# Optimization experiments

Measured on AMD Instinct MI355X. Metric: run time of the kernel, lower is better.

## Reference

```python
import jax, jax.numpy as jnp
import numpy as np

N, IN_F, OUT_F = 8192, 512, 256
ALPHA = 0.2  # leaky_relu negative slope
NEG_INF = -1e18


def setup_inputs() -> dict:
    key = jax.random.key(0)
    k1, k2, k3, k4 = jax.random.split(key, 4)
    h = jax.random.normal(k1, (N, IN_F), dtype=jnp.float32)
    adj = jax.random.randint(k2, (N, N), 0, 2, dtype=jnp.int32)
    # W: Linear(in_features, out_features, bias=False); stored [in, out] for x @ W
    lim_w = float(np.sqrt(6.0 / (IN_F + OUT_F)))
    W = jax.random.uniform(k3, (IN_F, OUT_F), minval=-lim_w, maxval=lim_w, dtype=jnp.float32)
    # a_T: Linear(2*out_features, 1); split into a1 (for H1=Wh_i) and a2 (for H2=Wh_j)
    lim_a = float(np.sqrt(6.0 / (2 * OUT_F + 1)))
    a = jax.random.uniform(k4, (2 * OUT_F,), minval=-lim_a, maxval=lim_a, dtype=jnp.float32)
    a1, a2 = a[:OUT_F], a[OUT_F:]
    return {"h": h, "adj": adj, "W": W, "a1": a1, "a2": a2}


def reference(h, adj, W, a1, a2):
    Wh = h @ W  # [N, F]
    # e_ij = leaky_relu(a . [Wh_i, Wh_j]) = leaky_relu(Wh_i.a1 + Wh_j.a2)
    # (mathematically identical to repeat+cat+linear, without the [N,N,2F] tensor)
    src = Wh @ a1  # [N]
    dst = Wh @ a2  # [N]
    e = jax.nn.leaky_relu(src[:, None] + dst[None, :], negative_slope=ALPHA)  # [N, N]
    masked_e = jnp.where(adj > 0, e, jnp.float32(NEG_INF))
    attn = jax.nn.softmax(masked_e, axis=-1)  # [N, N]
    h_prime = attn @ Wh  # [N, F]
    return jax.nn.elu(h_prime)
```

## Files before the change

### kernel.cpp

```cpp
#include <hip/hip_runtime.h>
#include <hip/hip_bf16.h>

#define NN 8192
#define KIN 512
#define KOUT 256
#define ALPHA 0.2f
#define BK 64
#define ROWS 128
#define KQ (NN / 4)
#define NT4 (KQ / BK)

typedef __bf16 bf16x8 __attribute__((ext_vector_type(8)));
typedef float f32x4 __attribute__((ext_vector_type(4)));
typedef unsigned short ushort8_t __attribute__((ext_vector_type(8)));
typedef unsigned short ushort4_t __attribute__((ext_vector_type(4)));
typedef int int4v __attribute__((ext_vector_type(4)));

__device__ __forceinline__ float lrelu(float x) { return x > 0.f ? x : ALPHA * x; }

__device__ __forceinline__ unsigned short f2bf(float f) {
  union { float f; unsigned u; } v; v.f = f;
  unsigned r = v.u + 0x7fffu + ((v.u >> 16) & 1u);
  return (unsigned short)(r >> 16);
}

__device__ __forceinline__ unsigned cvt_pk_bf16(float lo, float hi) {
  unsigned r;
  asm("v_cvt_pk_bf16_f32 %0, %1, %2" : "=v"(r) : "v"(lo), "v"(hi));
  return r;
}

__global__ __launch_bounds__(512) void k_wh(const float* __restrict__ h,
                                            const float* __restrict__ W,
                                            const float* __restrict__ a1,
                                            const float* __restrict__ a2,
                                            unsigned short* __restrict__ WhB,
                                            float* __restrict__ src,
                                            float* __restrict__ dstv) {
  __shared__ float sA[16][36];
  __shared__ float sB[16][260];
  const int tid = threadIdx.x;
  const int wave = tid >> 6;
  const int lane = tid & 63;
  const int bm = blockIdx.x * 32;
  const int arow = tid >> 4;
  const int akk = tid & 15;
  const int bkr = tid >> 5;
  const int bc = (tid & 31) * 8;
  float acc[4][4] = {};
  for (int k0 = 0; k0 < KIN; k0 += 16) {
    float av = h[(size_t)(bm + arow) * KIN + k0 + akk];
    const float4* wp = (const float4*)(W + (size_t)(k0 + bkr) * KOUT + bc);
    float4 w0 = wp[0], w1 = wp[1];
    __syncthreads();
    sA[akk][arow] = av;
    *(float4*)&sB[bkr][bc] = w0;
    *(float4*)&sB[bkr][bc + 4] = w1;
    __syncthreads();
#pragma unroll
    for (int k = 0; k < 16; ++k) {
      float4 a4 = *(const float4*)&sA[k][wave * 4];
      float4 b4 = *(const float4*)&sB[k][lane * 4];
      float aa[4] = {a4.x, a4.y, a4.z, a4.w};
      float bb[4] = {b4.x, b4.y, b4.z, b4.w};
#pragma unroll
      for (int i = 0; i < 4; ++i)
#pragma unroll
        for (int jj = 0; jj < 4; ++jj)
          acc[i][jj] = fmaf(aa[i], bb[jj], acc[i][jj]);
    }
  }
  float4 a1v = *(const float4*)(a1 + lane * 4);
  float4 a2v = *(const float4*)(a2 + lane * 4);
  float sp[4], dp[4];
#pragma unroll
  for (int i = 0; i < 4; ++i) {
    sp[i] = acc[i][0] * a1v.x + acc[i][1] * a1v.y + acc[i][2] * a1v.z + acc[i][3] * a1v.w;
    dp[i] = acc[i][0] * a2v.x + acc[i][1] * a2v.y + acc[i][2] * a2v.z + acc[i][3] * a2v.w;
  }
#pragma unroll
  for (int off = 32; off >= 1; off >>= 1) {
#pragma unroll
    for (int i = 0; i < 4; ++i) {
      sp[i] += __shfl_xor(sp[i], off);
      dp[i] += __shfl_xor(dp[i], off);
    }
  }
  if (lane == 0) {
#pragma unroll
    for (int i = 0; i < 4; ++i) {
      src[bm + wave * 4 + i] = sp[i];
      dstv[bm + wave * 4 + i] = dp[i];
    }
  }
#pragma unroll
  for (int i = 0; i < 4; ++i) {
    ushort4_t pk;
#pragma unroll
    for (int jj = 0; jj < 4; ++jj) pk[jj] = f2bf(acc[i][jj]);
    *(ushort4_t*)(WhB + (size_t)(bm + wave * 4 + i) * KOUT + lane * 4) = pk;
  }
}

__global__ __launch_bounds__(256) void k_trF(const unsigned short* __restrict__ WhB,
                                             unsigned short* __restrict__ WhF) {
  __shared__ unsigned int sX[64][65];
  const int t = threadIdx.x;
  const int r0 = (blockIdx.x & 127) * 64;
  const int c0 = (blockIdx.x >> 7) * 64;
  const int rr = t >> 2;
  const int cq = (t & 3) * 16;
  const ushort8_t* p = (const ushort8_t*)(WhB + (size_t)(r0 + rr) * KOUT + c0 + cq);
  ushort8_t v0 = p[0], v1 = p[1];
#pragma unroll
  for (int i = 0; i < 8; ++i) {
    sX[rr][cq + i] = v0[i];
    sX[rr][cq + 8 + i] = v1[i];
  }
  __syncthreads();
  const int wv = t >> 6;
  const int lane = t & 63;
  const int q = lane >> 4;
  const int fr = lane & 15;
  const int kt = r0 >> 6;
  const int wbase = c0 >> 5;
#pragma unroll
  for (int i = 0; i < 2; ++i) {
    const int g = wv * 2 + i;
    const int wloc = g >> 2;
    const int nc = (g >> 1) & 1;
    const int kh = g & 1;
    const int j0 = kh * 32 + q * 8;
    const int lc = wloc * 32 + nc * 16 + fr;
    ushort8_t o;
#pragma unroll
    for (int e = 0; e < 8; ++e) o[e] = (unsigned short)sX[j0 + e][lc];
    const int w = wbase + wloc;
    const size_t idx = ((((size_t)kt * 8 + w) * 2 + nc) * 2 + kh) * 64 + lane;
    *(ushort8_t*)(WhF + idx * 8) = o;
  }
}

__global__ __launch_bounds__(256) void k_dmax(const float* __restrict__ dstv,
                                              float* __restrict__ Dp) {
  __shared__ float red[256];
  const int t = threadIdx.x;
  float m = -3e38f;
  for (int i = t; i < NN; i += 256) m = fmaxf(m, dstv[i]);
  red[t] = m;
  __syncthreads();
  for (int s = 128; s >= 1; s >>= 1) {
    if (t < s) red[t] = fmaxf(red[t], red[t + s]);
    __syncthreads();
  }
  if (t == 0) *Dp = red[0];
}

struct Bset { ushort8_t b[2][2]; };

#define MF(a, b, c) __builtin_amdgcn_mfma_f32_16x16x32_bf16(a, b, c, 0, 0, 0)

#define BAR()                                              \
  {                                                        \
    asm volatile("s_waitcnt lgkmcnt(0)" ::: "memory");     \
    __builtin_amdgcn_s_barrier();                          \
    asm volatile("" ::: "memory");                         \
  }

#define TI(t) (((t) + ph0) & (NT4 - 1))

#define LOADB(BS, ktl)                                                 \
  {                                                                    \
    const unsigned short* p_ = bfw + (size_t)(ktl) * 16384;            \
    BS.b[0][0] = *(const ushort8_t*)(p_);                              \
    BS.b[0][1] = *(const ushort8_t*)(p_ + 512);                        \
    BS.b[1][0] = *(const ushort8_t*)(p_ + 1024);                       \
    BS.b[1][1] = *(const ushort8_t*)(p_ + 1536);                       \
  }

#define WGEN4(AJ, ktl, koff, buf)                                      \
  {                                                                    \
    float4 dv = *(const float4*)&sD[(ktl) * BK + (koff)];              \
    float x0 = s_r + dv.x, x1 = s_r + dv.y;                            \
    float x2 = s_r + dv.z, x3 = s_r + dv.w;                            \
    float w0 = (AJ.x > 0) ? __expf(fmaxf(x0, ALPHA * x0) - c_r) : 0.f; \
    float w1 = (AJ.y > 0) ? __expf(fmaxf(x1, ALPHA * x1) - c_r) : 0.f; \
    float w2 = (AJ.z > 0) ? __expf(fmaxf(x2, ALPHA * x2) - c_r) : 0.f; \
    float w3 = (AJ.w > 0) ? __expf(fmaxf(x3, ALPHA * x3) - c_r) : 0.f; \
    lsum += (w0 + w1) + (w2 + w3);                                     \
    uint2 pk;                                                          \
    pk.x = cvt_pk_bf16(w0, w1);                                        \
    pk.y = cvt_pk_bf16(w2, w3);                                        \
    *(uint2*)(sAb + (buf) * 16384 +                                    \
              ((pr * 128 + (koff) * 2) ^ ((pr & 7) << 4))) = pk;       \
  }

#define WGEN16(A0, A1, A2, A3, ktl, buf)                               \
  {                                                                    \
    WGEN4(A0, ktl, pk16 + 0, buf);                                     \
    WGEN4(A1, ktl, pk16 + 4, buf);                                     \
    WGEN4(A2, ktl, pk16 + 8, buf);                                     \
    WGEN4(A3, ktl, pk16 + 12, buf);                                    \
  }

#define LOADADJ16(A0, A1, A2, A3, ktl)                                 \
  {                                                                    \
    const int4v* ap = (const int4v*)(adjp + (size_t)(ktl) * BK);       \
    A0 = __builtin_nontemporal_load(ap);                               \
    A1 = __builtin_nontemporal_load(ap + 1);                           \
    A2 = __builtin_nontemporal_load(ap + 2);                           \
    A3 = __builtin_nontemporal_load(ap + 3);                           \
  }

#define LDA(cur, mr, kk)                                                        \
  __builtin_bit_cast(bf16x8,                                                    \
    *(const ushort8_t*)(sAb + (cur) * 16384 +                                   \
      ((((mr) * 16 + fr) * 128 + (kk) * 64 + fq * 16) ^ ((fr & 7) << 4))))

#define MSTEP(cur, BS)                                                 \
  {                                                                    \
    _Pragma("unroll")                                                  \
    for (int mr = 0; mr < 8; ++mr) {                                   \
      bf16x8 a0 = LDA(cur, mr, 0), a1 = LDA(cur, mr, 1);               \
      acc[mr][0] = MF(a0, BS.b[0][0], acc[mr][0]);                     \
      acc[mr][0] = MF(a1, BS.b[0][1], acc[mr][0]);                     \
      acc[mr][1] = MF(a0, BS.b[1][0], acc[mr][1]);                     \
      acc[mr][1] = MF(a1, BS.b[1][1], acc[mr][1]);                     \
    }                                                                  \
  }

__global__ __launch_bounds__(1024) void k_attn(const int* __restrict__ adj,
                                               const unsigned short* __restrict__ WhF,
                                               const float* __restrict__ src,
                                               const float* __restrict__ dstv,
                                               const float* __restrict__ Dp,
                                               float* __restrict__ Pbuf,
                                               float* __restrict__ Lsum) {
  __shared__ unsigned short sA[2][ROWS][BK];
  __shared__ float sD[KQ];
  char* sAb = (char*)&sA[0][0][0];
  const int tid = threadIdx.x;
  const int lane = tid & 63;
  const int wave = tid >> 6;
  const int qtr = blockIdx.x & 3;
  const int rg = blockIdx.x >> 2;
  const int r0 = rg * ROWS;
  const int ph0 = rg & (NT4 - 1);
  const int kbase = qtr * KQ;
  const float D = *Dp;

  *(float2*)&sD[tid * 2] = *(const float2*)(dstv + kbase + tid * 2);
  __syncthreads();

  const int ptid = tid - 512;
  const int pr = ptid >> 2;
  const int pk16 = (ptid & 3) * 16;
  const float s_r = src[r0 + pr];
  const float c_r = lrelu(s_r + D);
  const int* adjp = adj + (size_t)(r0 + pr) * NN + kbase + pk16;
  float lsum = 0.f;

  const int fr = lane & 15;
  const int fq = lane >> 4;
  const unsigned short* bfw =
      WhF + ((size_t)(qtr * NT4) * 8 + wave) * 2048 + lane * 8;
  f32x4 acc[8][2];
#pragma unroll
  for (int mr = 0; mr < 8; ++mr) {
    acc[mr][0] = (f32x4){0.f, 0.f, 0.f, 0.f};
    acc[mr][1] = (f32x4){0.f, 0.f, 0.f, 0.f};
  }
  Bset B0, B1;
  int4v aA0, aA1, aA2, aA3;
  int4v aB0, aB1, aB2, aB3;

  if (wave >= 8) {
    int4v d0, d1, d2, d3;
    {
      const int4v* ap = (const int4v*)(adjp + (size_t)TI(0) * BK);
      d0 = ap[0]; d1 = ap[1]; d2 = ap[2]; d3 = ap[3];
    }
    WGEN16(d0, d1, d2, d3, TI(0), 0);
    LOADADJ16(aB0, aB1, aB2, aB3, TI(1));
    LOADADJ16(aA0, aA1, aA2, aA3, TI(2));
  } else {
    LOADB(B0, TI(0));
    LOADB(B1, TI(1));
  }
  BAR();

  if (wave < 8) {
#pragma unroll 1
    for (int p = 0; p < NT4; p += 2) {
      { MSTEP(0, B0); LOADB(B0, TI(p + 2)); BAR(); }
      { MSTEP(1, B1); LOADB(B1, TI(p + 3)); BAR(); }
    }
#pragma unroll
    for (int mr = 0; mr < 8; ++mr) {
#pragma unroll
      for (int r = 0; r < 4; ++r) {
        const int row = mr * 16 + fq * 4 + r;
#pragma unroll
        for (int nc = 0; nc < 2; ++nc) {
          const int col = wave * 32 + nc * 16 + fr;
          Pbuf[(size_t)(qtr * NN + r0 + row) * KOUT + col] = acc[mr][nc][r];
        }
      }
    }
  } else {
#pragma unroll 1
    for (int p = 0; p < NT4; p += 2) {
      {
        WGEN16(aB0, aB1, aB2, aB3, TI(p + 1), 1);
        LOADADJ16(aB0, aB1, aB2, aB3, TI(p + 3));
        BAR();
      }
      {
        if (p + 2 < NT4) { WGEN16(aA0, aA1, aA2, aA3, TI(p + 2), 0); }
        LOADADJ16(aA0, aA1, aA2, aA3, TI(p + 4));
        BAR();
      }
    }
    lsum += __shfl_xor(lsum, 1, 4);
    lsum += __shfl_xor(lsum, 2, 4);
    if ((ptid & 3) == 0) Lsum[qtr * NN + r0 + pr] = lsum;
  }
}

__global__ __launch_bounds__(256) void k_comb(const float* __restrict__ Pbuf,
                                              const float* __restrict__ Lsum,
                                              float* __restrict__ out) {
  const int t = threadIdx.x;
  const int row = blockIdx.x * 4 + (t >> 6);
  const int col = (t & 63) * 4;
  const float l = Lsum[row] + Lsum[NN + row] + Lsum[2 * NN + row] + Lsum[3 * NN + row];
  float4 p0 = *(const float4*)(Pbuf + (size_t)row * KOUT + col);
  float4 p1 = *(const float4*)(Pbuf + (size_t)(NN + row) * KOUT + col);
  float4 p2 = *(const float4*)(Pbuf + (size_t)(2 * NN + row) * KOUT + col);
  float4 p3 = *(const float4*)(Pbuf + (size_t)(3 * NN + row) * KOUT + col);
  float4 v;
  v.x = (p0.x + p1.x + p2.x + p3.x) / l;
  v.y = (p0.y + p1.y + p2.y + p3.y) / l;
  v.z = (p0.z + p1.z + p2.z + p3.z) / l;
  v.w = (p0.w + p1.w + p2.w + p3.w) / l;
  v.x = v.x > 0.f ? v.x : __expf(v.x) - 1.f;
  v.y = v.y > 0.f ? v.y : __expf(v.y) - 1.f;
  v.z = v.z > 0.f ? v.z : __expf(v.z) - 1.f;
  v.w = v.w > 0.f ? v.w : __expf(v.w) - 1.f;
  *(float4*)(out + (size_t)row * KOUT + col) = v;
}

extern "C" void kernel_launch(void* const* d_in, const int* in_sizes, int n_in,
                              void* d_out, int out_size, void* d_ws, size_t ws_size,
                              hipStream_t stream) {
  const float* h = (const float*)d_in[0];
  const int* adj = (const int*)d_in[1];
  const float* W = (const float*)d_in[2];
  const float* a1 = (const float*)d_in[3];
  const float* a2 = (const float*)d_in[4];
  float* out = (float*)d_out;

  unsigned short* WhB = (unsigned short*)d_ws;
  unsigned short* WhF = WhB + (size_t)NN * KOUT;
  float* src = (float*)(WhF + (size_t)NN * KOUT);
  float* dstv = src + NN;
  float* Dp = dstv + NN;
  float* Pbuf = Dp + 16;
  float* Lsum = Pbuf + (size_t)4 * NN * KOUT;

  hipLaunchKernelGGL(k_wh, dim3(NN / 32), dim3(512), 0, stream, h, W, a1, a2, WhB, src, dstv);
  hipLaunchKernelGGL(k_trF, dim3(512), dim3(256), 0, stream, WhB, WhF);
  hipLaunchKernelGGL(k_dmax, dim3(1), dim3(256), 0, stream, dstv, Dp);
  hipLaunchKernelGGL(k_attn, dim3(256), dim3(1024), 0, stream, adj, WhF, src, dstv, Dp, Pbuf, Lsum);
  hipLaunchKernelGGL(k_comb, dim3(NN / 4), dim3(256), 0, stream, Pbuf, Lsum, out);
}
```

Measured before the change: 150.0 us.

## Factor softmax exponent into per-column and per-row terms; halve attention block size

The per-element exp(lrelu(s+d)-c) becomes max(exp(d)*exp(s-c), exp(alpha*d)*exp(alpha*s-c)). The per-column exponentials are precomputed into shared memory and the per-row factors into registers, so the inner weight generation needs only multiplies and a max instead of a transcendental per element. The block also shrinks from 1024 to 512 threads: 4 MFMA waves each own 64 output columns and 4 producer waves each handle 32 adjacent columns per row, with launch bounds asking for 2 blocks per CU. This trades more registers per wave and possible overflow or precision differences in the factored exponentials (exp(d) could overflow for large d) for less SFU work.

```diff
diff --git a/kernel.cpp b/kernel.cpp
--- a/kernel.cpp
+++ b/kernel.cpp
@@ -156,7 +156,7 @@
   if (t == 0) *Dp = red[0];
 }
 
-struct Bset { ushort8_t b[2][2]; };
+struct Bset { ushort8_t b[4][2]; };
 
 #define MF(a, b, c) __builtin_amdgcn_mfma_f32_16x16x32_bf16(a, b, c, 0, 0, 0)
 
@@ -176,17 +176,20 @@
     BS.b[0][1] = *(const ushort8_t*)(p_ + 512);                        \
     BS.b[1][0] = *(const ushort8_t*)(p_ + 1024);                       \
     BS.b[1][1] = *(const ushort8_t*)(p_ + 1536);                       \
+    BS.b[2][0] = *(const ushort8_t*)(p_ + 2048);                       \
+    BS.b[2][1] = *(const ushort8_t*)(p_ + 2560);                       \
+    BS.b[3][0] = *(const ushort8_t*)(p_ + 3072);                       \
+    BS.b[3][1] = *(const ushort8_t*)(p_ + 3584);                       \
   }
 
 #define WGEN4(AJ, ktl, koff, buf)                                      \
   {                                                                    \
-    float4 dv = *(const float4*)&sD[(ktl) * BK + (koff)];              \
-    float x0 = s_r + dv.x, x1 = s_r + dv.y;                            \
-    float x2 = s_r + dv.z, x3 = s_r + dv.w;                            \
-    float w0 = (AJ.x > 0) ? __expf(fmaxf(x0, ALPHA * x0) - c_r) : 0.f; \
-    float w1 = (AJ.y > 0) ? __expf(fmaxf(x1, ALPHA * x1) - c_r) : 0.f; \
-    float w2 = (AJ.z > 0) ? __expf(fmaxf(x2, ALPHA * x2) - c_r) : 0.f; \
-    float w3 = (AJ.w > 0) ? __expf(fmaxf(x3, ALPHA * x3) - c_r) : 0.f; \
+    float4 e1 = *(const float4*)&sE1[(ktl) * BK + (koff)];             \
+    float4 e2 = *(const float4*)&sE2[(ktl) * BK + (koff)];             \
+    float w0 = (AJ.x > 0) ? fmaxf(e1.x * F1, e2.x * F2) : 0.f;         \
+    float w1 = (AJ.y > 0) ? fmaxf(e1.y * F1, e2.y * F2) : 0.f;         \
+    float w2 = (AJ.z > 0) ? fmaxf(e1.z * F1, e2.z * F2) : 0.f;         \
+    float w3 = (AJ.w > 0) ? fmaxf(e1.w * F1, e2.w * F2) : 0.f;         \
     lsum += (w0 + w1) + (w2 + w3);                                     \
     uint2 pk;                                                          \
     pk.x = cvt_pk_bf16(w0, w1);                                        \
@@ -195,21 +198,17 @@
               ((pr * 128 + (koff) * 2) ^ ((pr & 7) << 4))) = pk;       \
   }
 
-#define WGEN16(A0, A1, A2, A3, ktl, buf)                               \
-  {                                                                    \
-    WGEN4(A0, ktl, pk16 + 0, buf);                                     \
-    WGEN4(A1, ktl, pk16 + 4, buf);                                     \
-    WGEN4(A2, ktl, pk16 + 8, buf);                                     \
-    WGEN4(A3, ktl, pk16 + 12, buf);                                    \
-  }
-
-#define LOADADJ16(A0, A1, A2, A3, ktl)                                 \
+#define WGEN32(R, ktl, buf)                                            \
+  {                                                                    \
+    _Pragma("unroll")                                                  \
+    for (int q = 0; q < 8; ++q) { WGEN4(R[q], ktl, pk32 + q * 4, buf); } \
+  }
+
+#define LOADADJ32(R, ktl)                                              \
   {                                                                    \
     const int4v* ap = (const int4v*)(adjp + (size_t)(ktl) * BK);       \
-    A0 = __builtin_nontemporal_load(ap);                               \
-    A1 = __builtin_nontemporal_load(ap + 1);                           \
-    A2 = __builtin_nontemporal_load(ap + 2);                           \
-    A3 = __builtin_nontemporal_load(ap + 3);                           \
+    _Pragma("unroll")                                                  \
+    for (int q = 0; q < 8; ++q) { R[q] = __builtin_nontemporal_load(ap + q); } \
   }
 
 #define LDA(cur, mr, kk)                                                        \
@@ -222,22 +221,24 @@
     _Pragma("unroll")                                                  \
     for (int mr = 0; mr < 8; ++mr) {                                   \
       bf16x8 a0 = LDA(cur, mr, 0), a1 = LDA(cur, mr, 1);               \
-      acc[mr][0] = MF(a0, BS.b[0][0], acc[mr][0]);                     \
-      acc[mr][0] = MF(a1, BS.b[0][1], acc[mr][0]);                     \
-      acc[mr][1] = MF(a0, BS.b[1][0], acc[mr][1]);                     \
-      acc[mr][1] = MF(a1, BS.b[1][1], acc[mr][1]);                     \
+      _Pragma("unroll")                                                \
+      for (int nc = 0; nc < 4; ++nc) {                                 \
+        acc[mr][nc] = MF(a0, BS.b[nc][0], acc[mr][nc]);                \
+        acc[mr][nc] = MF(a1, BS.b[nc][1], acc[mr][nc]);                \
+      }                                                                \
     }                                                                  \
   }
 
-__global__ __launch_bounds__(1024) void k_attn(const int* __restrict__ adj,
-                                               const unsigned short* __restrict__ WhF,
-                                               const float* __restrict__ src,
-                                               const float* __restrict__ dstv,
-                                               const float* __restrict__ Dp,
-                                               float* __restrict__ Pbuf,
-                                               float* __restrict__ Lsum) {
+__global__ __launch_bounds__(512, 2) void k_attn(const int* __restrict__ adj,
+                                                 const unsigned short* __restrict__ WhF,
+                                                 const float* __restrict__ src,
+                                                 const float* __restrict__ dstv,
+                                                 const float* __restrict__ Dp,
+                                                 float* __restrict__ Pbuf,
+                                                 float* __restrict__ Lsum) {
   __shared__ unsigned short sA[2][ROWS][BK];
-  __shared__ float sD[KQ];
+  __shared__ float sE1[KQ];
+  __shared__ float sE2[KQ];
   char* sAb = (char*)&sA[0][0][0];
   const int tid = threadIdx.x;
   const int lane = tid & 63;
@@ -249,51 +250,60 @@
   const int kbase = qtr * KQ;
   const float D = *Dp;
 
-  *(float2*)&sD[tid * 2] = *(const float2*)(dstv + kbase + tid * 2);
+  {
+    float4 d4 = *(const float4*)(dstv + kbase + tid * 4);
+    float4 t1, t2;
+    t1.x = __expf(d4.x); t1.y = __expf(d4.y); t1.z = __expf(d4.z); t1.w = __expf(d4.w);
+    t2.x = __expf(ALPHA * d4.x); t2.y = __expf(ALPHA * d4.y);
+    t2.z = __expf(ALPHA * d4.z); t2.w = __expf(ALPHA * d4.w);
+    *(float4*)&sE1[tid * 4] = t1;
+    *(float4*)&sE2[tid * 4] = t2;
+  }
   __syncthreads();
 
-  const int ptid = tid - 512;
-  const int pr = ptid >> 2;
-  const int pk16 = (ptid & 3) * 16;
+  const int ptid = tid - 256;
+  const int pr = ptid >> 1;
+  const int pk32 = (ptid & 1) * 32;
   const float s_r = src[r0 + pr];
   const float c_r = lrelu(s_r + D);
-  const int* adjp = adj + (size_t)(r0 + pr) * NN + kbase + pk16;
+  const float F1 = __expf(s_r - c_r);
+  const float F2 = __expf(ALPHA * s_r - c_r);
+  const int* adjp = adj + (size_t)(r0 + pr) * NN + kbase + pk32;
   float lsum = 0.f;
 
   const int fr = lane & 15;
   const int fq = lane >> 4;
   const unsigned short* bfw =
-      WhF + ((size_t)(qtr * NT4) * 8 + wave) * 2048 + lane * 8;
-  f32x4 acc[8][2];
-#pragma unroll
-  for (int mr = 0; mr < 8; ++mr) {
-    acc[mr][0] = (f32x4){0.f, 0.f, 0.f, 0.f};
-    acc[mr][1] = (f32x4){0.f, 0.f, 0.f, 0.f};
-  }
+      WhF + ((size_t)(qtr * NT4) * 8 + wave * 2) * 2048 + lane * 8;
+  f32x4 acc[8][4];
+#pragma unroll
+  for (int mr = 0; mr < 8; ++mr)
+#pragma unroll
+    for (int nc = 0; nc < 4; ++nc) acc[mr][nc] = (f32x4){0.f, 0.f, 0.f, 0.f};
   Bset B0, B1;
-  int4v aA0, aA1, aA2, aA3;
-  int4v aB0, aB1, aB2, aB3;
-
-  if (wave >= 8) {
-    int4v d0, d1, d2, d3;
+  int4v aA[8], aB[8];
+
+  if (wave >= 4) {
+    int4v d[8];
     {
       const int4v* ap = (const int4v*)(adjp + (size_t)TI(0) * BK);
-      d0 = ap[0]; d1 = ap[1]; d2 = ap[2]; d3 = ap[3];
-    }
-    WGEN16(d0, d1, d2, d3, TI(0), 0);
-    LOADADJ16(aB0, aB1, aB2, aB3, TI(1));
-    LOADADJ16(aA0, aA1, aA2, aA3, TI(2));
+#pragma unroll
+      for (int q = 0; q < 8; ++q) d[q] = ap[q];
+    }
+    WGEN32(d, TI(0), 0);
+    LOADADJ32(aB, TI(1));
+    LOADADJ32(aA, TI(2));
   } else {
     LOADB(B0, TI(0));
     LOADB(B1, TI(1));
   }
   BAR();
 
-  if (wave < 8) {
+  if (wave < 4) {
 #pragma unroll 1
     for (int p = 0; p < NT4; p += 2) {
-      { MSTEP(0, B0); LOADB(B0, TI(p + 2)); BAR(); }
-      { MSTEP(1, B1); LOADB(B1, TI(p + 3)); BAR(); }
+      { MSTEP(0, B0); LOADB(B0, TI(p + 2 < NT4 ? p + 2 : NT4 - 1)); BAR(); }
+      { MSTEP(1, B1); LOADB(B1, TI(p + 3 < NT4 ? p + 3 : NT4 - 1)); BAR(); }
     }
 #pragma unroll
     for (int mr = 0; mr < 8; ++mr) {
@@ -301,8 +311,8 @@
       for (int r = 0; r < 4; ++r) {
         const int row = mr * 16 + fq * 4 + r;
 #pragma unroll
-        for (int nc = 0; nc < 2; ++nc) {
-          const int col = wave * 32 + nc * 16 + fr;
+        for (int nc = 0; nc < 4; ++nc) {
+          const int col = wave * 64 + nc * 16 + fr;
           Pbuf[(size_t)(qtr * NN + r0 + row) * KOUT + col] = acc[mr][nc][r];
         }
       }
@@ -311,19 +321,18 @@
 #pragma unroll 1
     for (int p = 0; p < NT4; p += 2) {
       {
-        WGEN16(aB0, aB1, aB2, aB3, TI(p + 1), 1);
-        LOADADJ16(aB0, aB1, aB2, aB3, TI(p + 3));
+        WGEN32(aB, TI(p + 1), 1);
+        LOADADJ32(aB, TI(p + 3 < NT4 ? p + 3 : NT4 - 1));
         BAR();
       }
       {
-        if (p + 2 < NT4) { WGEN16(aA0, aA1, aA2, aA3, TI(p + 2), 0); }
-        LOADADJ16(aA0, aA1, aA2, aA3, TI(p + 4));
+        if (p + 2 < NT4) { WGEN32(aA, TI(p + 2), 0); }
+        LOADADJ32(aA, TI(p + 4 < NT4 ? p + 4 : NT4 - 1));
         BAR();
       }
     }
-    lsum += __shfl_xor(lsum, 1, 4);
-    lsum += __shfl_xor(lsum, 2, 4);
-    if ((ptid & 3) == 0) Lsum[qtr * NN + r0 + pr] = lsum;
+    lsum += __shfl_xor(lsum, 1, 2);
+    if ((ptid & 1) == 0) Lsum[qtr * NN + r0 + pr] = lsum;
   }
 }
 
@@ -371,6 +380,6 @@
   hipLaunchKernelGGL(k_wh, dim3(NN / 32), dim3(512), 0, stream, h, W, a1, a2, WhB, src, dstv);
   hipLaunchKernelGGL(k_trF, dim3(512), dim3(256), 0, stream, WhB, WhF);
   hipLaunchKernelGGL(k_dmax, dim3(1), dim3(256), 0, stream, dstv, Dp);
-  hipLaunchKernelGGL(k_attn, dim3(256), dim3(1024), 0, stream, adj, WhF, src, dstv, Dp, Pbuf, Lsum);
+  hipLaunchKernelGGL(k_attn, dim3(256), dim3(512), 0, stream, adj, WhF, src, dstv, Dp, Pbuf, Lsum);
   hipLaunchKernelGGL(k_comb, dim3(NN / 4), dim3(256), 0, stream, Pbuf, Lsum, out);
 }
```

Measured after the change: 193.7 us. +29.2%, slower.

## Move Wh projection to bf16 MFMA and fold attention scores and max into it

Applied to the files above, without the earlier changes.

Replaces the scalar-FMA fp32 h@W kernel with an MFMA bf16 GEMM. W is pre-converted to bf16 in fragment layout, and h is converted on the fly into swizzled shared memory. The src/dst scores are computed as h·(W a1) and h·(W a2) from small precomputed vectors. The global max of dst is taken with an order-preserving atomicMax, which removes the single-block k_dmax reduction kernel. This trades extra bf16 rounding of h and W for lower compute time in the projection stage, and adds two small prep kernels.

```diff
diff --git a/kernel.cpp b/kernel.cpp
--- a/kernel.cpp
+++ b/kernel.cpp
@@ -13,7 +13,6 @@
 typedef __bf16 bf16x8 __attribute__((ext_vector_type(8)));
 typedef float f32x4 __attribute__((ext_vector_type(4)));
 typedef unsigned short ushort8_t __attribute__((ext_vector_type(8)));
-typedef unsigned short ushort4_t __attribute__((ext_vector_type(4)));
 typedef int int4v __attribute__((ext_vector_type(4)));
 
 __device__ __forceinline__ float lrelu(float x) { return x > 0.f ? x : ALPHA * x; }
@@ -30,75 +29,171 @@
   return r;
 }
 
-__global__ __launch_bounds__(512) void k_wh(const float* __restrict__ h,
-                                            const float* __restrict__ W,
+__device__ __forceinline__ unsigned fkey(float x) {
+  unsigned b = __float_as_uint(x);
+  return (b & 0x80000000u) ? ~b : (b | 0x80000000u);
+}
+__device__ __forceinline__ float funkey(unsigned k) {
+  unsigned b = (k & 0x80000000u) ? (k ^ 0x80000000u) : ~k;
+  return __uint_as_float(b);
+}
+
+#define MF(a, b, c) __builtin_amdgcn_mfma_f32_16x16x32_bf16(a, b, c, 0, 0, 0)
+
+__global__ __launch_bounds__(256) void k_wa(const float* __restrict__ W,
                                             const float* __restrict__ a1,
                                             const float* __restrict__ a2,
-                                            unsigned short* __restrict__ WhB,
-                                            float* __restrict__ src,
-                                            float* __restrict__ dstv) {
-  __shared__ float sA[16][36];
-  __shared__ float sB[16][260];
+                                            float* __restrict__ Wa1,
+                                            float* __restrict__ Wa2,
+                                            unsigned* __restrict__ Dup) {
+  const int k = blockIdx.x * 256 + threadIdx.x;
+  float s1 = 0.f, s2 = 0.f;
+  const float* wr = W + (size_t)k * KOUT;
+  for (int c = 0; c < KOUT; c += 4) {
+    float4 w4 = *(const float4*)(wr + c);
+    float4 b1 = *(const float4*)(a1 + c);
+    float4 b2 = *(const float4*)(a2 + c);
+    s1 += w4.x * b1.x + w4.y * b1.y + w4.z * b1.z + w4.w * b1.w;
+    s2 += w4.x * b2.x + w4.y * b2.y + w4.z * b2.z + w4.w * b2.w;
+  }
+  Wa1[k] = s1;
+  Wa2[k] = s2;
+  if (k == 0) *Dup = 0u;
+}
+
+__global__ __launch_bounds__(64) void k_prep(const float* __restrict__ W,
+                                             unsigned short* __restrict__ Wb) {
+  const int b = blockIdx.x;
+  const int kt = b >> 4, cg = b & 15;
+  const int l = threadIdx.x;
+  const int krow = kt * 32 + (l >> 4) * 8;
+  const int col = cg * 16 + (l & 15);
+  ushort8_t o;
+#pragma unroll
+  for (int e = 0; e < 8; ++e) o[e] = f2bf(W[(size_t)(krow + e) * KOUT + col]);
+  *(ushort8_t*)(Wb + ((size_t)b * 64 + l) * 8) = o;
+}
+
+__global__ __launch_bounds__(512) void k_wh2(const float* __restrict__ h,
+                                             const unsigned short* __restrict__ Wb,
+                                             const float* __restrict__ Wa1,
+                                             const float* __restrict__ Wa2,
+                                             unsigned short* __restrict__ WhB,
+                                             float* __restrict__ src,
+                                             float* __restrict__ dstv,
+                                             unsigned* __restrict__ Dup) {
+  __shared__ unsigned short sH[64][64];
+  __shared__ unsigned short sBounce[64][128];
+  __shared__ float sW1[KIN], sW2[KIN];
+  char* sHb = (char*)&sH[0][0];
   const int tid = threadIdx.x;
-  const int wave = tid >> 6;
   const int lane = tid & 63;
-  const int bm = blockIdx.x * 32;
-  const int arow = tid >> 4;
-  const int akk = tid & 15;
-  const int bkr = tid >> 5;
-  const int bc = (tid & 31) * 8;
-  float acc[4][4] = {};
-  for (int k0 = 0; k0 < KIN; k0 += 16) {
-    float av = h[(size_t)(bm + arow) * KIN + k0 + akk];
-    const float4* wp = (const float4*)(W + (size_t)(k0 + bkr) * KOUT + bc);
-    float4 w0 = wp[0], w1 = wp[1];
+  const int wv = tid >> 6;
+  const int r0 = blockIdx.x * 64;
+  const int fr = lane & 15, fq = lane >> 4;
+
+  sW1[tid] = Wa1[tid];
+  sW2[tid] = Wa2[tid];
+
+  const int srow = tid >> 3;
+  const int skc = (tid & 7) * 8;
+  const float* hp = h + (size_t)(r0 + srow) * KIN + skc;
+  const int wby = ((srow * 128 + skc * 2) ^ ((srow & 7) << 4));
+  float sp = 0.f, dp = 0.f;
+
+  f32x4 acc[4][2];
+#pragma unroll
+  for (int mr = 0; mr < 4; ++mr) {
+    acc[mr][0] = (f32x4){0.f, 0.f, 0.f, 0.f};
+    acc[mr][1] = (f32x4){0.f, 0.f, 0.f, 0.f};
+  }
+  ushort8_t Bs[2][2];
+
+  float hv[8];
+  {
+    float4 a = *(const float4*)hp;
+    float4 b = *(const float4*)(hp + 4);
+    hv[0] = a.x; hv[1] = a.y; hv[2] = a.z; hv[3] = a.w;
+    hv[4] = b.x; hv[5] = b.y; hv[6] = b.z; hv[7] = b.w;
+  }
+
+#pragma unroll 1
+  for (int it = 0; it < 8; ++it) {
     __syncthreads();
-    sA[akk][arow] = av;
-    *(float4*)&sB[bkr][bc] = w0;
-    *(float4*)&sB[bkr][bc + 4] = w1;
+    const int kb = it * 64 + skc;
+#pragma unroll
+    for (int j = 0; j < 8; ++j) {
+      sp = fmaf(hv[j], sW1[kb + j], sp);
+      dp = fmaf(hv[j], sW2[kb + j], dp);
+    }
+    uint4 pk;
+    pk.x = cvt_pk_bf16(hv[0], hv[1]);
+    pk.y = cvt_pk_bf16(hv[2], hv[3]);
+    pk.z = cvt_pk_bf16(hv[4], hv[5]);
+    pk.w = cvt_pk_bf16(hv[6], hv[7]);
+    *(uint4*)(sHb + wby) = pk;
+    float hn[8];
+    if (it < 7) {
+      float4 a = *(const float4*)(hp + (it + 1) * 64);
+      float4 b = *(const float4*)(hp + (it + 1) * 64 + 4);
+      hn[0] = a.x; hn[1] = a.y; hn[2] = a.z; hn[3] = a.w;
+      hn[4] = b.x; hn[5] = b.y; hn[6] = b.z; hn[7] = b.w;
+    }
     __syncthreads();
 #pragma unroll
-    for (int k = 0; k < 16; ++k) {
-      float4 a4 = *(const float4*)&sA[k][wave * 4];
-      float4 b4 = *(const float4*)&sB[k][lane * 4];
-      float aa[4] = {a4.x, a4.y, a4.z, a4.w};
-      float bb[4] = {b4.x, b4.y, b4.z, b4.w};
-#pragma unroll
-      for (int i = 0; i < 4; ++i)
-#pragma unroll
-        for (int jj = 0; jj < 4; ++jj)
-          acc[i][jj] = fmaf(aa[i], bb[jj], acc[i][jj]);
-    }
-  }
-  float4 a1v = *(const float4*)(a1 + lane * 4);
-  float4 a2v = *(const float4*)(a2 + lane * 4);
-  float sp[4], dp[4];
-#pragma unroll
-  for (int i = 0; i < 4; ++i) {
-    sp[i] = acc[i][0] * a1v.x + acc[i][1] * a1v.y + acc[i][2] * a1v.z + acc[i][3] * a1v.w;
-    dp[i] = acc[i][0] * a2v.x + acc[i][1] * a2v.y + acc[i][2] * a2v.z + acc[i][3] * a2v.w;
-  }
-#pragma unroll
-  for (int off = 32; off >= 1; off >>= 1) {
-#pragma unroll
-    for (int i = 0; i < 4; ++i) {
-      sp[i] += __shfl_xor(sp[i], off);
-      dp[i] += __shfl_xor(dp[i], off);
-    }
-  }
-  if (lane == 0) {
-#pragma unroll
-    for (int i = 0; i < 4; ++i) {
-      src[bm + wave * 4 + i] = sp[i];
-      dstv[bm + wave * 4 + i] = dp[i];
-    }
-  }
-#pragma unroll
-  for (int i = 0; i < 4; ++i) {
-    ushort4_t pk;
-#pragma unroll
-    for (int jj = 0; jj < 4; ++jj) pk[jj] = f2bf(acc[i][jj]);
-    *(ushort4_t*)(WhB + (size_t)(bm + wave * 4 + i) * KOUT + lane * 4) = pk;
+    for (int n = 0; n < 2; ++n)
+#pragma unroll
+      for (int kk = 0; kk < 2; ++kk)
+        Bs[n][kk] = *(const ushort8_t*)(Wb +
+            (((size_t)(it * 2 + kk) * 16 + wv * 2 + n) * 64 + lane) * 8);
+#pragma unroll
+    for (int mr = 0; mr < 4; ++mr) {
+      bf16x8 a0 = __builtin_bit_cast(bf16x8, *(const ushort8_t*)(sHb +
+          (((mr * 16 + fr) * 128 + 0 * 64 + fq * 16) ^ ((fr & 7) << 4))));
+      bf16x8 a1 = __builtin_bit_cast(bf16x8, *(const ushort8_t*)(sHb +
+          (((mr * 16 + fr) * 128 + 1 * 64 + fq * 16) ^ ((fr & 7) << 4))));
+      acc[mr][0] = MF(a0, Bs[0][0], acc[mr][0]);
+      acc[mr][0] = MF(a1, Bs[0][1], acc[mr][0]);
+      acc[mr][1] = MF(a0, Bs[1][0], acc[mr][1]);
+      acc[mr][1] = MF(a1, Bs[1][1], acc[mr][1]);
+    }
+#pragma unroll
+    for (int j = 0; j < 8; ++j) hv[j] = hn[j];
+  }
+
+  sp += __shfl_xor(sp, 1, 8);
+  sp += __shfl_xor(sp, 2, 8);
+  sp += __shfl_xor(sp, 4, 8);
+  dp += __shfl_xor(dp, 1, 8);
+  dp += __shfl_xor(dp, 2, 8);
+  dp += __shfl_xor(dp, 4, 8);
+  if ((tid & 7) == 0) {
+    src[r0 + srow] = sp;
+    dstv[r0 + srow] = dp;
+    atomicMax(Dup, fkey(dp));
+  }
+
+#pragma unroll 1
+  for (int pass = 0; pass < 2; ++pass) {
+    __syncthreads();
+    if ((wv >> 2) == pass) {
+      const int fbase = (wv & 3) * 32;
+#pragma unroll
+      for (int mr = 0; mr < 4; ++mr)
+#pragma unroll
+        for (int n = 0; n < 2; ++n)
+#pragma unroll
+          for (int r = 0; r < 4; ++r)
+            sBounce[mr * 16 + fq * 4 + r][fbase + n * 16 + fr] =
+                f2bf(acc[mr][n][r]);
+    }
+    __syncthreads();
+    const int crow = tid >> 3;
+    const int cfo = (tid & 7) * 16;
+    *(ushort8_t*)(WhB + (size_t)(r0 + crow) * KOUT + pass * 128 + cfo) =
+        *(const ushort8_t*)&sBounce[crow][cfo];
+    *(ushort8_t*)(WhB + (size_t)(r0 + crow) * KOUT + pass * 128 + cfo + 8) =
+        *(const ushort8_t*)&sBounce[crow][cfo + 8];
   }
 }
 
@@ -141,24 +236,7 @@
   }
 }
 
-__global__ __launch_bounds__(256) void k_dmax(const float* __restrict__ dstv,
-                                              float* __restrict__ Dp) {
-  __shared__ float red[256];
-  const int t = threadIdx.x;
-  float m = -3e38f;
-  for (int i = t; i < NN; i += 256) m = fmaxf(m, dstv[i]);
-  red[t] = m;
-  __syncthreads();
-  for (int s = 128; s >= 1; s >>= 1) {
-    if (t < s) red[t] = fmaxf(red[t], red[t + s]);
-    __syncthreads();
-  }
-  if (t == 0) *Dp = red[0];
-}
-
 struct Bset { ushort8_t b[2][2]; };
-
-#define MF(a, b, c) __builtin_amdgcn_mfma_f32_16x16x32_bf16(a, b, c, 0, 0, 0)
 
 #define BAR()                                              \
   {                                                        \
@@ -233,7 +311,7 @@
                                                const unsigned short* __restrict__ WhF,
                                                const float* __restrict__ src,
                                                const float* __restrict__ dstv,
-                                               const float* __restrict__ Dp,
+                                               const unsigned* __restrict__ Dup,
                                                float* __restrict__ Pbuf,
                                                float* __restrict__ Lsum) {
   __shared__ unsigned short sA[2][ROWS][BK];
@@ -247,7 +325,7 @@
   const int r0 = rg * ROWS;
   const int ph0 = rg & (NT4 - 1);
   const int kbase = qtr * KQ;
-  const float D = *Dp;
+  const float D = funkey(*Dup);
 
   *(float2*)&sD[tid * 2] = *(const float2*)(dstv + kbase + tid * 2);
   __syncthreads();
@@ -364,13 +442,19 @@
   unsigned short* WhF = WhB + (size_t)NN * KOUT;
   float* src = (float*)(WhF + (size_t)NN * KOUT);
   float* dstv = src + NN;
-  float* Dp = dstv + NN;
-  float* Pbuf = Dp + 16;
+  unsigned* Dup = (unsigned*)(dstv + NN);
+  float* Pbuf = (float*)(Dup + 16);
   float* Lsum = Pbuf + (size_t)4 * NN * KOUT;
-
-  hipLaunchKernelGGL(k_wh, dim3(NN / 32), dim3(512), 0, stream, h, W, a1, a2, WhB, src, dstv);
+  unsigned short* Wb = (unsigned short*)(Lsum + 4 * NN);
+  float* Wa1 = (float*)(Wb + (size_t)KIN * KOUT);
+  float* Wa2 = Wa1 + KIN;
+
+  hipLaunchKernelGGL(k_wa, dim3(2), dim3(256), 0, stream, W, a1, a2, Wa1, Wa2, Dup);
+  hipLaunchKernelGGL(k_prep, dim3(256), dim3(64), 0, stream, W, Wb);
+  hipLaunchKernelGGL(k_wh2, dim3(NN / 64), dim3(512), 0, stream,
+                     h, Wb, Wa1, Wa2, WhB, src, dstv, Dup);
   hipLaunchKernelGGL(k_trF, dim3(512), dim3(256), 0, stream, WhB, WhF);
-  hipLaunchKernelGGL(k_dmax, dim3(1), dim3(256), 0, stream, dstv, Dp);
-  hipLaunchKernelGGL(k_attn, dim3(256), dim3(1024), 0, stream, adj, WhF, src, dstv, Dp, Pbuf, Lsum);
+  hipLaunchKernelGGL(k_attn, dim3(256), dim3(1024), 0, stream,
+                     adj, WhF, src, dstv, Dup, Pbuf, Lsum);
   hipLaunchKernelGGL(k_comb, dim3(NN / 4), dim3(256), 0, stream, Pbuf, Lsum, out);
 }
```

Measured after the change: 138.7 us. 7.5% less time.
